# Kernel optimization log

Measured on AMD Instinct MI355X. Metric: run time of the kernel, lower is better.

The kernel has to match this reference:

```python
import jax, jax.numpy as jnp
import numpy as np

K_LO, K_HI = 5, 3
HAM_LO = jnp.asarray(np.outer(np.hamming(K_LO), np.hamming(K_LO)), dtype=jnp.float32)
HAM_HI = jnp.asarray(np.outer(np.hamming(K_HI), np.hamming(K_HI)), dtype=jnp.float32)


def conv2d(x, w, b, pad):
    y = jax.lax.conv_general_dilated(x, w, (1, 1), [(pad, pad), (pad, pad)],
                                     dimension_numbers=('NCHW', 'OIHW', 'NCHW'))
    return y + b[None, :, None, None]


def kernel_normalizer(mask, k, ham):
    # softmax over k*k, modulate by hamming window, renormalize to sum 1
    n, mc, h, w = mask.shape
    ch = mc // (k * k)
    m = jax.nn.softmax(mask.reshape(n, ch, k * k, h, w), axis=2)
    m = m.reshape(n, ch, k, k, h, w) * ham[None, None, :, :, None, None]
    m = m / m.sum(axis=(2, 3), keepdims=True)
    return m.reshape(n, mc, h, w)


def extract_patches(x, k):
    # (n,c,h,w) -> (n,c,k*k,h,w), zero-padded, row-major kernel order (matches CARAFE)
    n, c, h, w = x.shape
    p = k // 2
    xp = jnp.pad(x, ((0, 0), (0, 0), (p, p), (p, p)))
    return jnp.stack([xp[:, :, i:i + h, j:j + w] for i in range(k) for j in range(k)], axis=2)


def carafe(x, mask, k, group, up):
    # content-aware reassembly: mask is at (h*up, w*up); source pixel = out_pixel // up
    n, c, h, w = x.shape
    cg = c // group
    patches = extract_patches(x, k).reshape(n, group, cg, k * k, h, w)
    if up == 1:
        m = mask.reshape(n, group, k * k, h, w)
        return jnp.einsum('ngckhw,ngkhw->ngchw', patches, m).reshape(n, c, h, w)
    m = mask.reshape(n, group, k * k, h, up, w, up)
    out = jnp.einsum('ngckhw,ngkhuwv->ngchuwv', patches, m)
    return out.reshape(n, c, h * up, w * up)


def _forward(hr_feat, lr_feat, W_hr, b_hr, W_lr, b_lr, W_enc, b_enc, W_enc2, b_enc2):
    chf = conv2d(hr_feat, W_hr, b_hr, 0)
    clf = conv2d(lr_feat, W_lr, b_lr, 0)
    mask_hr_hr = conv2d(chf, W_enc2, b_enc2, 1)
    m_hi = kernel_normalizer(mask_hr_hr, K_HI, HAM_HI)
    chf = 2.0 * chf - carafe(chf, m_hi, K_HI, 1, 1)
    mask_lr_hr = conv2d(chf, W_enc, b_enc, 1)
    m_lo = kernel_normalizer(mask_lr_hr, K_LO, HAM_LO)
    # carafe(up=2) output is already at hr resolution -> F.interpolate(nearest) is identity
    mask_lr_lr = carafe(conv2d(clf, W_enc, b_enc, 1), m_lo, K_LO, 1, 2)
    mask_lr = mask_lr_hr + mask_lr_lr
    m_lo2 = kernel_normalizer(mask_lr, K_LO, HAM_LO)
    mask_hr_lr = carafe(conv2d(clf, W_enc2, b_enc2, 1), m_lo2, K_LO, 1, 2)
    mask_hr = mask_hr_hr + mask_hr_lr
    mask_lr_n = kernel_normalizer(mask_lr, K_LO, HAM_LO)
    lr_out = carafe(lr_feat, mask_lr_n, K_LO, 1, 2)
    mask_hr_n = kernel_normalizer(mask_hr, K_HI, HAM_HI)
    hr_out = 2.0 * hr_feat - carafe(hr_feat, mask_hr_n, K_HI, 1, 1)
    return (mask_lr_n, hr_out, lr_out)


def setup_inputs() -> dict:
    key = jax.random.key(0)
    ks = jax.random.split(key, 10)
    B, CHR, CLR, CC = 2, 256, 256, 64
    H, W = 128, 128
    h, w = H // 2, W // 2
    f32 = jnp.float32
    return {
        'hr_feat': jax.random.normal(ks[0], (B, CHR, H, W), f32),
        'lr_feat': jax.random.normal(ks[1], (B, CLR, h, w), f32),
        'W_hr': jax.random.normal(ks[2], (CC, CHR, 1, 1), f32) * 0.05,
        'b_hr': jnp.zeros((CC,), f32),
        'W_lr': jax.random.normal(ks[3], (CC, CLR, 1, 1), f32) * 0.05,
        'b_lr': jnp.zeros((CC,), f32),
        'W_enc': jax.random.normal(ks[4], (K_LO * K_LO, CC, 3, 3), f32) * 0.001,
        'b_enc': jnp.zeros((K_LO * K_LO,), f32),
        'W_enc2': jax.random.normal(ks[5], (K_HI * K_HI, CC, 3, 3), f32) * 0.001,
        'b_enc2': jnp.zeros((K_HI * K_HI,), f32),
    }


def reference(hr_feat, lr_feat, W_hr, b_hr, W_lr, b_lr, W_enc, b_enc, W_enc2, b_enc2):
    return _forward(hr_feat, lr_feat, W_hr, b_hr, W_lr, b_lr, W_enc, b_enc, W_enc2, b_enc2)
```

## Files before the change

### kernel.cpp

```cpp
#include <hip/hip_runtime.h>

#define HWH 16384
#define HWL 4096
#define WH 128
#define WL 64

__device__ __forceinline__ float ham3v(int t) {
    const float h[3] = {0.08f, 1.0f, 0.08f};
    return h[t / 3] * h[t % 3];
}
__device__ __forceinline__ float ham5v(int t) {
    const float h[5] = {0.08f, 0.54f, 1.0f, 0.54f, 0.08f};
    return h[t / 5] * h[t % 5];
}

template <int K>
__device__ __forceinline__ void normalize_post(float* m) {
    constexpr int K2 = K * K;
    float mx = -1e30f;
#pragma unroll
    for (int k = 0; k < K2; k++) mx = fmaxf(mx, m[k]);
    float s = 0.f;
#pragma unroll
    for (int k = 0; k < K2; k++) {
        float hv = (K == 3) ? ham3v(k) : ham5v(k);
        float e = __expf(m[k] - mx) * hv;
        m[k] = e;
        s += e;
    }
    float inv = 1.f / s;
#pragma unroll
    for (int k = 0; k < K2; k++) m[k] *= inv;
}

template <int K>
__device__ __forceinline__ void normalize_mask(const float* __restrict src, int stride,
                                               float* m) {
#pragma unroll
    for (int k = 0; k < K * K; k++) m[k] = src[(size_t)k * stride];
    normalize_post<K>(m);
}

struct F4 { float x, y, z, w; };
__device__ __forceinline__ F4 ld4u(const float* p) {
    F4 v;
    __builtin_memcpy(&v, p, 16);
    return v;
}

__device__ __forceinline__ float4 add4(float4 a, float4 b) {
    return make_float4(a.x + b.x, a.y + b.y, a.z + b.z, a.w + b.w);
}

__global__ void prep_w_k(const float* __restrict Whr, const float* __restrict Wlr,
                         const float* __restrict Wenc, const float* __restrict Wenc2,
                         float* __restrict wbase) {
    int tid = blockIdx.x * blockDim.x + threadIdx.x;
    int stride = gridDim.x * blockDim.x;
    float* wt_hr = wbase;
    float* wt_lr = wbase + 16384;
    float* wtE = wbase + 32768;
    float* wtE2 = wbase + 51200;
    for (int i = tid; i < 16384; i += stride) {
        int ci = i >> 6, co = i & 63;
        wt_hr[i] = Whr[co * 256 + ci];
        wt_lr[i] = Wlr[co * 256 + ci];
    }
    for (int i = tid; i < 18432; i += stride) {
        int r = i >> 5, co = i & 31;
        int ci = r / 9, t = r % 9;
        wtE[i] = (co < 25) ? Wenc[(co * 64 + ci) * 9 + t] : 0.f;
    }
    for (int i = tid; i < 9216; i += stride) {
        int r = i >> 4, co = i & 15;
        int ci = r / 9, t = r % 9;
        wtE2[i] = (co < 9) ? Wenc2[(co * 64 + ci) * 9 + t] : 0.f;
    }
}

__global__ __launch_bounds__(512) void conv1x1_all_k(
    const float* __restrict hr, const float* __restrict lrf, const float* __restrict wt_hr,
    const float* __restrict wt_lr, const float* __restrict bhr, const float* __restrict blr,
    float* __restrict chf, float* __restrict clf, int N) {
    __shared__ float sm[128 * 128];
    int b = blockIdx.x;
    const int HRB = (HWH / 128) * N;
    const float *x, *wt, *bias;
    float* y;
    int HWp, n, px0;
    if (b < HRB) {
        x = hr; wt = wt_hr; bias = bhr; y = chf; HWp = HWH;
        n = b / (HWH / 128);
        px0 = (b % (HWH / 128)) * 128;
    } else {
        int b2 = b - HRB;
        x = lrf; wt = wt_lr; bias = blr; y = clf; HWp = HWL;
        n = b2 / (HWL / 128);
        px0 = (b2 % (HWL / 128)) * 128;
    }
    const float* xb = x + (size_t)n * 256 * HWp + px0;
    int pl = threadIdx.x & 127;
    int co0 = __builtin_amdgcn_readfirstlane((int)(threadIdx.x >> 7)) * 16;
    float acc[16];
#pragma unroll
    for (int j = 0; j < 16; j++) acc[j] = 0.f;
    const float* w0 = wt + co0;
#pragma unroll
    for (int half = 0; half < 2; half++) {
        __syncthreads();
        for (int e = threadIdx.x; e < 4096; e += 512) {
            int ci = e >> 5, q = e & 31;
            *reinterpret_cast<float4*>(sm + ci * 128 + q * 4) =
                *reinterpret_cast<const float4*>(xb + (size_t)(half * 128 + ci) * HWp + q * 4);
        }
        __syncthreads();
        const float* wh = w0 + (half * 128) * 64;
#pragma unroll 8
        for (int ci = 0; ci < 128; ci++) {
            float xv = sm[ci * 128 + pl];
            const float* wr = wh + ci * 64;
#pragma unroll
            for (int j = 0; j < 16; j++) acc[j] = fmaf(wr[j], xv, acc[j]);
        }
    }
    float* yb = y + ((size_t)(n * 64 + co0)) * HWp + px0 + pl;
#pragma unroll
    for (int j = 0; j < 16; j++) yb[(size_t)j * HWp] = acc[j] + bias[co0 + j];
}

template <int COUT, int CH, int PAD, int LOG2W, int HH, int WW, int NCI>
__device__ __forceinline__ void conv3x3_2px(const float* __restrict x,
                                            const float* __restrict wt,
                                            const float* __restrict bias,
                                            float* __restrict y, int n, int g, int pxh,
                                            int ci0, bool addb) {
    constexpr int HWp = HH * WW;
    int px = pxh * 2;
    int yy = px >> LOG2W, xx = px & (WW - 1);
    int co0 = g * CH;
    float a0[CH], a1[CH];
#pragma unroll
    for (int j = 0; j < CH; j++) { a0[j] = 0.f; a1[j] = 0.f; }
    const float* xb = x + (size_t)(n * 64 + ci0) * HWp;
    const float* wb0 = wt + (size_t)ci0 * 9 * PAD + co0;
    int roff[3];
    bool rv[3];
#pragma unroll
    for (int r = 0; r < 3; r++) {
        int sy = yy + r - 1;
        rv[r] = (sy >= 0) && (sy < HH);
        roff[r] = sy * WW + xx - 1;
    }
    bool lv = (xx > 0), rgv = (xx < WW - 2);
    for (int ci = 0; ci < NCI; ci++) {
        const float* xc = xb + (size_t)ci * HWp;
        const float* w = wb0 + (size_t)ci * 9 * PAD;
#pragma unroll
        for (int r = 0; r < 3; r++) {
            F4 v = ld4u(xc + roff[r]);
            float t0 = (rv[r] && lv) ? v.x : 0.f;
            float t1 = rv[r] ? v.y : 0.f;
            float t2 = rv[r] ? v.z : 0.f;
            float t3 = (rv[r] && rgv) ? v.w : 0.f;
#pragma unroll
            for (int j = 0; j < CH; j++) {
                float w0 = w[(r * 3 + 0) * PAD + j];
                float w1 = w[(r * 3 + 1) * PAD + j];
                float w2 = w[(r * 3 + 2) * PAD + j];
                a0[j] = fmaf(w0, t0, fmaf(w1, t1, fmaf(w2, t2, a0[j])));
                a1[j] = fmaf(w0, t1, fmaf(w1, t2, fmaf(w2, t3, a1[j])));
            }
        }
    }
#pragma unroll
    for (int j = 0; j < CH; j++) {
        int co = co0 + j;
        if (co < COUT) {
            float bv = addb ? bias[co] : 0.f;
            float* op = y + ((size_t)(n * COUT + co)) * HWp + px;
            *reinterpret_cast<float2*>(op) = make_float2(a0[j] + bv, a1[j] + bv);
        }
    }
}

__global__ __launch_bounds__(256) void conv3x3_CGK_k(
    const float* __restrict chf, const float* __restrict clf, const float* __restrict wtE,
    const float* __restrict wtE2, const float* __restrict benc,
    const float* __restrict benc2, float* __restrict mh_P, float* __restrict g_P,
    float* __restrict k_P, int N) {
    const size_t MS = (size_t)N * 9 * HWH, GS = (size_t)N * 25 * HWL,
                 KS = (size_t)N * 9 * HWL;
    const int GBl = 8 * N * 5 * 4, KBl = 8 * N * 2 * 4;
    int b = blockIdx.x;
    if (b < GBl) {
        int pxb = b % 8;
        int n = (b / 8) % N;
        int t = b / (8 * N);
        int g = t % 5, s = t / 5;
        conv3x3_2px<25, 5, 32, 6, WL, WL, 16>(clf, wtE, benc, g_P + s * GS, n, g,
                                              pxb * 256 + (int)threadIdx.x, s * 16, s == 0);
    } else if (b < GBl + KBl) {
        int b2 = b - GBl;
        int pxb = b2 % 8;
        int n = (b2 / 8) % N;
        int t = b2 / (8 * N);
        int g = t % 2, s = t / 2;
        conv3x3_2px<9, 5, 16, 6, WL, WL, 16>(clf, wtE2, benc2, k_P + s * KS, n, g,
                                             pxb * 256 + (int)threadIdx.x, s * 16, s == 0);
    } else {
        int b3 = b - GBl - KBl;
        int pxb = b3 % 32;
        int n = (b3 / 32) % N;
        int t = b3 / (32 * N);
        int g = t % 3, s = t / 3;
        conv3x3_2px<9, 3, 16, 7, WH, WH, 16>(chf, wtE2, benc2, mh_P + s * MS, n, g,
                                             pxb * 256 + (int)threadIdx.x, s * 16, s == 0);
    }
}

__global__ __launch_bounds__(256) void conv3x3_F_k(const float* __restrict chf2,
                                                   const float* __restrict wtE,
                                                   const float* __restrict benc,
                                                   float* __restrict mlr_P, int N) {
    const size_t FS = (size_t)N * 25 * HWH;
    int t = blockIdx.x;
    int pxb = t % 32; t /= 32;
    int n = t % N; t /= N;
    int g = t % 5;
    int s = t / 5;
    conv3x3_2px<25, 5, 32, 7, WH, WH, 16>(chf2, wtE, benc, mlr_P + s * FS, n, g,
                                          pxb * 256 + (int)threadIdx.x, s * 16, s == 0);
}

__global__ void sum4n_gkc_k(const float* __restrict mh_P, float* __restrict mh_sum,
                            float* __restrict mh_n, const float4* __restrict g,
                            float4* __restrict g_d, const float4* __restrict k,
                            float4* __restrict k_d, int N) {
    const int NA = N * HWH / 256;
    const int E2 = N * 25 * HWL / 4, E3 = N * 9 * HWL / 4;
    const int NB = E2 / 256;
    const size_t MS = (size_t)N * 9 * HWH;
    int b = blockIdx.x;
    if (b < NA) {
        int lin = b * 256 + threadIdx.x;
        int n = lin / HWH, px = lin % HWH;
        float m[9];
#pragma unroll
        for (int c = 0; c < 9; c++) {
            size_t o = ((size_t)n * 9 + c) * HWH + px;
            float s = mh_P[o] + mh_P[o + MS] + mh_P[o + 2 * MS] + mh_P[o + 3 * MS];
            m[c] = s;
            mh_sum[o] = s;
        }
        normalize_post<3>(m);
#pragma unroll
        for (int c = 0; c < 9; c++) mh_n[((size_t)n * 9 + c) * HWH + px] = m[c];
    } else if (b < NA + NB) {
        int i = (b - NA) * 256 + threadIdx.x;
        if (i < E2) g_d[i] = add4(add4(g[i], g[i + E2]), add4(g[i + 2 * E2], g[i + 3 * E2]));
    } else {
        int i = (b - NA - NB) * 256 + threadIdx.x;
        if (i < E3) k_d[i] = add4(add4(k[i], k[i + E3]), add4(k[i + 2 * E3], k[i + 3 * E3]));
    }
}

__global__ void sum4fn_k(const float* __restrict p, float* __restrict sum,
                         float* __restrict nrm, int N) {
    int lin = blockIdx.x * 64 + threadIdx.x;
    int n = lin / HWH, px = lin % HWH;
    const size_t FS = (size_t)N * 25 * HWH;
    float m[25];
#pragma unroll
    for (int c = 0; c < 25; c++) {
        size_t o = ((size_t)n * 25 + c) * HWH + px;
        float s = p[o] + p[o + FS] + p[o + 2 * FS] + p[o + 3 * FS];
        sum[o] = s;
        m[c] = s;
    }
    normalize_post<5>(m);
    float* np = nrm + (size_t)n * 25 * HWH + px;
#pragma unroll
    for (int c = 0; c < 25; c++) np[(size_t)c * HWH] = m[c];
}

__device__ __forceinline__ void stage_tile18(const float* __restrict src,
                                             float (*__restrict tile)[18][136], int y0) {
    int tid = threadIdx.x;
    if (tid < 144) {
        int r = tid >> 3, c8 = tid & 7;
        int col = (c8 < 4) ? c8 : 128 + c8;
#pragma unroll
        for (int c = 0; c < 4; c++) tile[c][r][col] = 0.f;
    }
#pragma unroll
    for (int c = 0; c < 4; c++) {
        const float* sp = src + (size_t)c * HWH;
#pragma unroll
        for (int p = 0; p < 3; p++) {
            int e = tid + p * 256;
            if (e < 576) {
                int r = e >> 5, q = e & 31;
                int gy = y0 + r - 1;
                float4 v = make_float4(0.f, 0.f, 0.f, 0.f);
                if (gy >= 0 && gy < WH) v = *(const float4*)(sp + gy * WH + q * 4);
                *(float4*)&tile[c][r][4 + q * 4] = v;
            }
        }
    }
    __syncthreads();
}

template <bool SUBTRACT>
__device__ __forceinline__ void carafe3_tile8(const float (*__restrict tile)[18][136],
                                              const float* __restrict mb, int y0,
                                              float* __restrict ob) {
    int ly = threadIdx.x >> 4;
    int x0 = (threadIdx.x & 15) * 8;
    int px = (y0 + ly) * WH + x0;
    float4 ma[9], mbv[9];
#pragma unroll
    for (int t = 0; t < 9; t++) {
        ma[t] = *(const float4*)(mb + (size_t)t * HWH + px);
        mbv[t] = *(const float4*)(mb + (size_t)t * HWH + px + 4);
    }
    for (int c = 0; c < 4; c++) {
        float row[3][10];
#pragma unroll
        for (int r = 0; r < 3; r++) {
            const float* tp = &tile[c][ly + r][0];
            float lft = tp[3 + x0];
            float4 m0 = *(const float4*)&tp[4 + x0];
            float4 m1 = *(const float4*)&tp[8 + x0];
            float rgt = tp[12 + x0];
            row[r][0] = lft;
            row[r][1] = m0.x; row[r][2] = m0.y; row[r][3] = m0.z; row[r][4] = m0.w;
            row[r][5] = m1.x; row[r][6] = m1.y; row[r][7] = m1.z; row[r][8] = m1.w;
            row[r][9] = rgt;
        }
        float4 resA, resB;
        float* rp = &resA.x;
        float* rq = &resB.x;
#pragma unroll
        for (int p = 0; p < 8; p++) {
            float s = 0.f;
#pragma unroll
            for (int r = 0; r < 3; r++)
#pragma unroll
                for (int cc = 0; cc < 3; cc++) {
                    float mv = (p < 4) ? ((const float*)&ma[r * 3 + cc])[p]
                                       : ((const float*)&mbv[r * 3 + cc])[p - 4];
                    s = fmaf(mv, row[r][p + cc], s);
                }
            float o = SUBTRACT ? (2.f * row[1][p + 1] - s) : s;
            if (p < 4) rp[p] = o; else rq[p - 4] = o;
        }
        float* op = ob + (size_t)c * HWH + px;
        *(float4*)op = resA;
        *(float4*)(op + 4) = resB;
    }
}

__global__ __launch_bounds__(256) void fuse_de_k(const float* __restrict chf,
                                                 const float* __restrict m9n,
                                                 float* __restrict chf2, int N) {
    __shared__ float tile[4][18][136];
    int b = blockIdx.x;
    int yt = b & 7;
    int g = (b >> 3) & 15;
    int n = b >> 7;
    int y0 = yt * 16;
    int c0 = g * 4;
    stage_tile18(chf + ((size_t)n * 64 + c0) * HWH, tile, y0);
    carafe3_tile8<true>(tile, m9n + (size_t)n * 9 * HWH, y0,
                        chf2 + ((size_t)n * 64 + c0) * HWH);
}

__global__ void fuse_hi_k(const float* __restrict msum, const float* __restrict mn,
                          const float* __restrict g, float* __restrict mask_lr, int N) {
    int b = blockIdx.x;
    int pxb = b % 64;
    int n = (b / 64) % N;
    int co0 = (b / (64 * N)) * 5;
    int px = pxb * 256 + threadIdx.x;
    int Y = px >> 7, X = px & 127;
    int h = Y >> 1, w = X >> 1;
    const float* mb = msum + (size_t)n * 25 * HWH + px;
    const float* nb = mn + (size_t)n * 25 * HWH + px;
    float ml[25];
#pragma unroll
    for (int k = 0; k < 25; k++) ml[k] = nb[(size_t)k * HWH];
    float acc[5];
#pragma unroll
    for (int j = 0; j < 5; j++) acc[j] = 0.f;
    const float* gb = g + ((size_t)n * 25 + co0) * HWL;
    for (int k = 0; k < 25; k++) {
        int sy = h + k / 5 - 2, sx = w + k % 5 - 2;
        if (sy >= 0 && sy < WL && sx >= 0 && sx < WL) {
            int off = sy * WL + sx;
            float mk = ml[k];
#pragma unroll
            for (int j = 0; j < 5; j++)
                acc[j] = fmaf(mk, gb[(size_t)j * HWL + off], acc[j]);
        }
    }
#pragma unroll
    for (int j = 0; j < 5; j++)
        mask_lr[((size_t)(n * 25 + co0 + j)) * HWH + px] =
            mb[(size_t)(co0 + j) * HWH] + acc[j];
}

__global__ void fuse_l_norm_k(const float* __restrict mask_lr, const float* __restrict kf,
                              const float* __restrict mh_sum, float* __restrict out0,
                              float* __restrict mask_hr_n, int N) {
    int b = blockIdx.x;
    int px = (b % 256) * 64 + threadIdx.x;
    int n = b / 256;
    int Y = px >> 7, X = px & 127;
    int h = Y >> 1, w = X >> 1;
    float ml[25];
    normalize_mask<5>(mask_lr + (size_t)n * 25 * HWH + px, HWH, ml);
    float* op = out0 + (size_t)n * 25 * HWH + px;
#pragma unroll
    for (int k = 0; k < 25; k++) op[(size_t)k * HWH] = ml[k];
    float acc[9];
#pragma unroll
    for (int j = 0; j < 9; j++) acc[j] = 0.f;
    const float* kb = kf + (size_t)n * 9 * HWL;
    for (int k = 0; k < 25; k++) {
        int sy = h + k / 5 - 2, sx = w + k % 5 - 2;
        if (sy >= 0 && sy < WL && sx >= 0 && sx < WL) {
            int off = sy * WL + sx;
            float mk = ml[k];
#pragma unroll
            for (int j = 0; j < 9; j++)
                acc[j] = fmaf(mk, kb[(size_t)j * HWL + off], acc[j]);
        }
    }
    float mh[9];
#pragma unroll
    for (int j = 0; j < 9; j++)
        mh[j] = mh_sum[((size_t)(n * 9 + j)) * HWH + px] + acc[j];
    normalize_post<3>(mh);
    float* dp = mask_hr_n + (size_t)n * 9 * HWH + px;
#pragma unroll
    for (int j = 0; j < 9; j++) dp[(size_t)j * HWH] = mh[j];
}

__global__ __launch_bounds__(256) void hr_out_k(const float* __restrict m9n,
                                                const float* __restrict hr,
                                                float* __restrict out1, int N) {
    __shared__ float tile[4][18][136];
    int b = blockIdx.x;
    int yt = b & 7;
    int g = (b >> 3) & 63;
    int n = b >> 9;
    int y0 = yt * 16;
    int c0 = g * 4;
    stage_tile18(hr + ((size_t)n * 256 + c0) * HWH, tile, y0);
    carafe3_tile8<true>(tile, m9n + (size_t)n * 9 * HWH, y0,
                        out1 + ((size_t)n * 256 + c0) * HWH);
}

#define LRCHG 8
__global__ __launch_bounds__(256) void lr_out_k(const float* __restrict m_n,
                                                const float* __restrict lr,
                                                float* __restrict out2, int N) {
    __shared__ float tile[LRCHG][12][68];
    int b = blockIdx.x;
    int yt = b & 7;
    int g = (b >> 3) & 31;
    int n = b >> 8;
    int y0 = yt * 16;
    int hbase = y0 >> 1;
    int c0 = g * LRCHG;
    const float* lrb = lr + ((size_t)n * 256 + c0) * HWL;
    if (threadIdx.x < 48) {
        int r = threadIdx.x >> 2, c4 = threadIdx.x & 3;
        int col = (c4 < 2) ? c4 : 64 + c4;
#pragma unroll
        for (int c = 0; c < LRCHG; c++) tile[c][r][col] = 0.f;
    }
#pragma unroll
    for (int c = 0; c < LRCHG; c++) {
        const float* sp = lrb + (size_t)c * HWL;
#pragma unroll
        for (int p = 0; p < 2; p++) {
            int e = threadIdx.x + p * 256;
            if (e < 384) {
                int r = e >> 5, q = e & 31;
                int h = hbase + r - 2;
                float2 v = make_float2(0.f, 0.f);
                if (h >= 0 && h < WL) v = *(const float2*)(sp + h * WL + q * 2);
                *(float2*)&tile[c][r][2 + q * 2] = v;
            }
        }
    }
    __syncthreads();
    const float* mb = m_n + (size_t)n * 25 * HWH;
    float* ob = out2 + ((size_t)n * 256 + c0) * HWH;
#pragma unroll
    for (int i = 0; i < 2; i++) {
        int q = threadIdx.x + 256 * i;
        int qy = q >> 6, qx = q & 63;
        int Y0 = y0 + 2 * qy;
        int X0 = 2 * qx;
        float2 mk0[25], mk1[25];
#pragma unroll
        for (int k = 0; k < 25; k++) {
            mk0[k] = *(const float2*)(mb + (size_t)k * HWH + Y0 * WH + X0);
            mk1[k] = *(const float2*)(mb + (size_t)k * HWH + (Y0 + 1) * WH + X0);
        }
        for (int c = 0; c < LRCHG; c++) {
            float a00 = 0.f, a01 = 0.f, a10 = 0.f, a11 = 0.f;
#pragma unroll
            for (int k = 0; k < 25; k++) {
                float v = tile[c][qy + k / 5][qx + k % 5];
                a00 = fmaf(mk0[k].x, v, a00);
                a01 = fmaf(mk0[k].y, v, a01);
                a10 = fmaf(mk1[k].x, v, a10);
                a11 = fmaf(mk1[k].y, v, a11);
            }
            float* op = ob + (size_t)c * HWH + (size_t)Y0 * WH + X0;
            *(float2*)op = make_float2(a00, a01);
            *(float2*)(op + WH) = make_float2(a10, a11);
        }
    }
}

extern "C" void kernel_launch(void* const* d_in, const int* in_sizes, int n_in, void* d_out,
                              int out_size, void* d_ws, size_t ws_size, hipStream_t stream) {
    const float* hr = (const float*)d_in[0];
    const float* lr = (const float*)d_in[1];
    const float* Whr = (const float*)d_in[2];
    const float* bhr = (const float*)d_in[3];
    const float* Wlr = (const float*)d_in[4];
    const float* blr = (const float*)d_in[5];
    const float* Wenc = (const float*)d_in[6];
    const float* benc = (const float*)d_in[7];
    const float* Wenc2 = (const float*)d_in[8];
    const float* benc2 = (const float*)d_in[9];
    float* out = (float*)d_out;
    const int B = in_sizes[0] / (256 * HWH);
    (void)d_ws; (void)ws_size;

    float* out0 = out;
    float* O1 = out + (size_t)B * 25 * HWH;
    float* O2 = O1 + (size_t)B * 256 * HWH;

    const size_t MS = (size_t)B * 9 * HWH;
    const size_t GS = (size_t)B * 25 * HWL;
    const size_t KS = (size_t)B * 9 * HWL;
    const size_t FS = (size_t)B * 25 * HWH;

    float* wbase = O2;
    float* wt_hr = wbase;
    float* wt_lr = wbase + 16384;
    float* wtE = wbase + 32768;
    float* wtE2 = wbase + 51200;
    float* mh_P = O2 + 60416;
    float* g_P = mh_P + 4 * MS;
    float* k_P = g_P + 4 * GS;
    float* m_hrhr_sum = k_P + 4 * KS;
    float* g_sum = m_hrhr_sum + MS;
    float* k_sum = g_sum + GS;
    float* m_lrhr_sum = k_sum + KS;
    float* mask_hr_n = m_lrhr_sum + FS;
    float* m_lrhr_n = mask_hr_n + MS;

    float* chf = O1;
    float* chf2 = chf + (size_t)B * 64 * HWH;
    float* clf = chf2 + (size_t)B * 64 * HWH;
    float* mlr_P = clf + (size_t)B * 64 * HWL;
    float* m_hrhr_n = mlr_P + 4 * FS;
    float* mask_lr = mlr_P;

    prep_w_k<<<64, 256, 0, stream>>>(Whr, Wlr, Wenc, Wenc2, wbase);
    conv1x1_all_k<<<(HWH / 128) * B + (HWL / 128) * B, 512, 0, stream>>>(
        hr, lr, wt_hr, wt_lr, bhr, blr, chf, clf, B);
    conv3x3_CGK_k<<<8 * B * 5 * 4 + 8 * B * 2 * 4 + 32 * B * 3 * 4, 256, 0, stream>>>(
        chf, clf, wtE, wtE2, benc, benc2, mh_P, g_P, k_P, B);
    {
        int NA = B * HWH / 256;
        int NB = (B * 25 * HWL / 4) / 256, NC = (B * 9 * HWL / 4) / 256;
        sum4n_gkc_k<<<NA + NB + NC, 256, 0, stream>>>(
            mh_P, m_hrhr_sum, m_hrhr_n, (const float4*)g_P, (float4*)g_sum,
            (const float4*)k_P, (float4*)k_sum, B);
    }
    fuse_de_k<<<B * 128, 256, 0, stream>>>(chf, m_hrhr_n, chf2, B);
    conv3x3_F_k<<<32 * B * 5 * 4, 256, 0, stream>>>(chf2, wtE, benc, mlr_P, B);
    sum4fn_k<<<B * HWH / 64, 64, 0, stream>>>(mlr_P, m_lrhr_sum, m_lrhr_n, B);
    fuse_hi_k<<<64 * B * 5, 256, 0, stream>>>(m_lrhr_sum, m_lrhr_n, g_sum, mask_lr, B);
    fuse_l_norm_k<<<256 * B, 64, 0, stream>>>(mask_lr, k_sum, m_hrhr_sum, out0, mask_hr_n,
                                              B);
    hr_out_k<<<B * 512, 256, 0, stream>>>(mask_hr_n, hr, O1, B);
    lr_out_k<<<B * 256, 256, 0, stream>>>(out0, lr, O2, B);
}
```

Before: 159.2 us.

## Merge hr/lr output kernels into one launch; halve conv1x1 block size

The hr_out and lr_out carafe kernels are combined into a single launch that picks its branch from the block index. To make this safe, the normalized hr mask moves from the O2 region, which lr_out overwrites, into the workspace. The old two-kernel path stays as a fallback when the workspace is too small. Separately, conv1x1 now uses 256-thread blocks over 64 pixels instead of 512 threads over 128, which doubles the block count and halves shared memory per block, trading some weight reuse for more occupancy.

```diff
diff --git a/kernel.cpp b/kernel.cpp
--- a/kernel.cpp
+++ b/kernel.cpp
@@ -78,29 +78,29 @@
     }
 }
 
-__global__ __launch_bounds__(512) void conv1x1_all_k(
+__global__ __launch_bounds__(256) void conv1x1_all_k(
     const float* __restrict hr, const float* __restrict lrf, const float* __restrict wt_hr,
     const float* __restrict wt_lr, const float* __restrict bhr, const float* __restrict blr,
     float* __restrict chf, float* __restrict clf, int N) {
-    __shared__ float sm[128 * 128];
+    __shared__ float sm[128 * 64];
     int b = blockIdx.x;
-    const int HRB = (HWH / 128) * N;
+    const int HRB = (HWH / 64) * N;
     const float *x, *wt, *bias;
     float* y;
     int HWp, n, px0;
     if (b < HRB) {
         x = hr; wt = wt_hr; bias = bhr; y = chf; HWp = HWH;
-        n = b / (HWH / 128);
-        px0 = (b % (HWH / 128)) * 128;
+        n = b / (HWH / 64);
+        px0 = (b % (HWH / 64)) * 64;
     } else {
         int b2 = b - HRB;
         x = lrf; wt = wt_lr; bias = blr; y = clf; HWp = HWL;
-        n = b2 / (HWL / 128);
-        px0 = (b2 % (HWL / 128)) * 128;
+        n = b2 / (HWL / 64);
+        px0 = (b2 % (HWL / 64)) * 64;
     }
     const float* xb = x + (size_t)n * 256 * HWp + px0;
-    int pl = threadIdx.x & 127;
-    int co0 = __builtin_amdgcn_readfirstlane((int)(threadIdx.x >> 7)) * 16;
+    int pl = threadIdx.x & 63;
+    int co0 = __builtin_amdgcn_readfirstlane((int)(threadIdx.x >> 6)) * 16;
     float acc[16];
 #pragma unroll
     for (int j = 0; j < 16; j++) acc[j] = 0.f;
@@ -108,16 +108,16 @@
 #pragma unroll
     for (int half = 0; half < 2; half++) {
         __syncthreads();
-        for (int e = threadIdx.x; e < 4096; e += 512) {
-            int ci = e >> 5, q = e & 31;
-            *reinterpret_cast<float4*>(sm + ci * 128 + q * 4) =
+        for (int e = threadIdx.x; e < 2048; e += 256) {
+            int ci = e >> 4, q = e & 15;
+            *reinterpret_cast<float4*>(sm + ci * 64 + q * 4) =
                 *reinterpret_cast<const float4*>(xb + (size_t)(half * 128 + ci) * HWp + q * 4);
         }
         __syncthreads();
         const float* wh = w0 + (half * 128) * 64;
 #pragma unroll 8
         for (int ci = 0; ci < 128; ci++) {
-            float xv = sm[ci * 128 + pl];
+            float xv = sm[ci * 64 + pl];
             const float* wr = wh + ci * 64;
 #pragma unroll
             for (int j = 0; j < 16; j++) acc[j] = fmaf(wr[j], xv, acc[j]);
@@ -360,6 +360,87 @@
     }
 }
 
+__device__ __forceinline__ void hr_out_body(float* __restrict smem,
+                                            const float* __restrict m9n,
+                                            const float* __restrict hr,
+                                            float* __restrict out1, int b, int N) {
+    float(*tile)[18][136] = reinterpret_cast<float(*)[18][136]>(smem);
+    int yt = b & 7;
+    int g = (b >> 3) & 63;
+    int n = b >> 9;
+    int y0 = yt * 16;
+    int c0 = g * 4;
+    stage_tile18(hr + ((size_t)n * 256 + c0) * HWH, tile, y0);
+    carafe3_tile8<true>(tile, m9n + (size_t)n * 9 * HWH, y0,
+                        out1 + ((size_t)n * 256 + c0) * HWH);
+}
+
+#define LRCHG 8
+__device__ __forceinline__ void lr_out_body(float* __restrict smem,
+                                            const float* __restrict m_n,
+                                            const float* __restrict lrf,
+                                            float* __restrict out2, int b, int N) {
+    float(*tile)[12][68] = reinterpret_cast<float(*)[12][68]>(smem);
+    int yt = b & 7;
+    int g = (b >> 3) & 31;
+    int n = b >> 8;
+    int y0 = yt * 16;
+    int hbase = y0 >> 1;
+    int c0 = g * LRCHG;
+    const float* lrb = lrf + ((size_t)n * 256 + c0) * HWL;
+    if (threadIdx.x < 48) {
+        int r = threadIdx.x >> 2, c4 = threadIdx.x & 3;
+        int col = (c4 < 2) ? c4 : 64 + c4;
+#pragma unroll
+        for (int c = 0; c < LRCHG; c++) tile[c][r][col] = 0.f;
+    }
+#pragma unroll
+    for (int c = 0; c < LRCHG; c++) {
+        const float* sp = lrb + (size_t)c * HWL;
+#pragma unroll
+        for (int p = 0; p < 2; p++) {
+            int e = threadIdx.x + p * 256;
+            if (e < 384) {
+                int r = e >> 5, q = e & 31;
+                int h = hbase + r - 2;
+                float2 v = make_float2(0.f, 0.f);
+                if (h >= 0 && h < WL) v = *(const float2*)(sp + h * WL + q * 2);
+                *(float2*)&tile[c][r][2 + q * 2] = v;
+            }
+        }
+    }
+    __syncthreads();
+    const float* mb = m_n + (size_t)n * 25 * HWH;
+    float* ob = out2 + ((size_t)n * 256 + c0) * HWH;
+#pragma unroll
+    for (int i = 0; i < 2; i++) {
+        int q = threadIdx.x + 256 * i;
+        int qy = q >> 6, qx = q & 63;
+        int Y0 = y0 + 2 * qy;
+        int X0 = 2 * qx;
+        float2 mk0[25], mk1[25];
+#pragma unroll
+        for (int k = 0; k < 25; k++) {
+            mk0[k] = *(const float2*)(mb + (size_t)k * HWH + Y0 * WH + X0);
+            mk1[k] = *(const float2*)(mb + (size_t)k * HWH + (Y0 + 1) * WH + X0);
+        }
+        for (int c = 0; c < LRCHG; c++) {
+            float a00 = 0.f, a01 = 0.f, a10 = 0.f, a11 = 0.f;
+#pragma unroll
+            for (int k = 0; k < 25; k++) {
+                float v = tile[c][qy + k / 5][qx + k % 5];
+                a00 = fmaf(mk0[k].x, v, a00);
+                a01 = fmaf(mk0[k].y, v, a01);
+                a10 = fmaf(mk1[k].x, v, a10);
+                a11 = fmaf(mk1[k].y, v, a11);
+            }
+            float* op = ob + (size_t)c * HWH + (size_t)Y0 * WH + X0;
+            *(float2*)op = make_float2(a00, a01);
+            *(float2*)(op + WH) = make_float2(a10, a11);
+        }
+    }
+}
+
 __global__ __launch_bounds__(256) void fuse_de_k(const float* __restrict chf,
                                                  const float* __restrict m9n,
                                                  float* __restrict chf2, int N) {
@@ -449,81 +530,30 @@
 __global__ __launch_bounds__(256) void hr_out_k(const float* __restrict m9n,
                                                 const float* __restrict hr,
                                                 float* __restrict out1, int N) {
-    __shared__ float tile[4][18][136];
+    __shared__ float smem[4 * 18 * 136];
+    hr_out_body(smem, m9n, hr, out1, blockIdx.x, N);
+}
+
+__global__ __launch_bounds__(256) void lr_out_k(const float* __restrict m_n,
+                                                const float* __restrict lrf,
+                                                float* __restrict out2, int N) {
+    __shared__ float smem[LRCHG * 12 * 68];
+    lr_out_body(smem, m_n, lrf, out2, blockIdx.x, N);
+}
+
+__global__ __launch_bounds__(256) void hrlr_out_k(const float* __restrict m9n,
+                                                  const float* __restrict hr,
+                                                  float* __restrict out1,
+                                                  const float* __restrict m_n,
+                                                  const float* __restrict lrf,
+                                                  float* __restrict out2, int N) {
+    __shared__ float smem[4 * 18 * 136];
     int b = blockIdx.x;
-    int yt = b & 7;
-    int g = (b >> 3) & 63;
-    int n = b >> 9;
-    int y0 = yt * 16;
-    int c0 = g * 4;
-    stage_tile18(hr + ((size_t)n * 256 + c0) * HWH, tile, y0);
-    carafe3_tile8<true>(tile, m9n + (size_t)n * 9 * HWH, y0,
-                        out1 + ((size_t)n * 256 + c0) * HWH);
-}
-
-#define LRCHG 8
-__global__ __launch_bounds__(256) void lr_out_k(const float* __restrict m_n,
-                                                const float* __restrict lr,
-                                                float* __restrict out2, int N) {
-    __shared__ float tile[LRCHG][12][68];
-    int b = blockIdx.x;
-    int yt = b & 7;
-    int g = (b >> 3) & 31;
-    int n = b >> 8;
-    int y0 = yt * 16;
-    int hbase = y0 >> 1;
-    int c0 = g * LRCHG;
-    const float* lrb = lr + ((size_t)n * 256 + c0) * HWL;
-    if (threadIdx.x < 48) {
-        int r = threadIdx.x >> 2, c4 = threadIdx.x & 3;
-        int col = (c4 < 2) ? c4 : 64 + c4;
-#pragma unroll
-        for (int c = 0; c < LRCHG; c++) tile[c][r][col] = 0.f;
-    }
-#pragma unroll
-    for (int c = 0; c < LRCHG; c++) {
-        const float* sp = lrb + (size_t)c * HWL;
-#pragma unroll
-        for (int p = 0; p < 2; p++) {
-            int e = threadIdx.x + p * 256;
-            if (e < 384) {
-                int r = e >> 5, q = e & 31;
-                int h = hbase + r - 2;
-                float2 v = make_float2(0.f, 0.f);
-                if (h >= 0 && h < WL) v = *(const float2*)(sp + h * WL + q * 2);
-                *(float2*)&tile[c][r][2 + q * 2] = v;
-            }
-        }
-    }
-    __syncthreads();
-    const float* mb = m_n + (size_t)n * 25 * HWH;
-    float* ob = out2 + ((size_t)n * 256 + c0) * HWH;
-#pragma unroll
-    for (int i = 0; i < 2; i++) {
-        int q = threadIdx.x + 256 * i;
-        int qy = q >> 6, qx = q & 63;
-        int Y0 = y0 + 2 * qy;
-        int X0 = 2 * qx;
-        float2 mk0[25], mk1[25];
-#pragma unroll
-        for (int k = 0; k < 25; k++) {
-            mk0[k] = *(const float2*)(mb + (size_t)k * HWH + Y0 * WH + X0);
-            mk1[k] = *(const float2*)(mb + (size_t)k * HWH + (Y0 + 1) * WH + X0);
-        }
-        for (int c = 0; c < LRCHG; c++) {
-            float a00 = 0.f, a01 = 0.f, a10 = 0.f, a11 = 0.f;
-#pragma unroll
-            for (int k = 0; k < 25; k++) {
-                float v = tile[c][qy + k / 5][qx + k % 5];
-                a00 = fmaf(mk0[k].x, v, a00);
-                a01 = fmaf(mk0[k].y, v, a01);
-                a10 = fmaf(mk1[k].x, v, a10);
-                a11 = fmaf(mk1[k].y, v, a11);
-            }
-            float* op = ob + (size_t)c * HWH + (size_t)Y0 * WH + X0;
-            *(float2*)op = make_float2(a00, a01);
-            *(float2*)(op + WH) = make_float2(a10, a11);
-        }
+    const int HRB = N * 512;
+    if (b < HRB) {
+        hr_out_body(smem, m9n, hr, out1, b, N);
+    } else {
+        lr_out_body(smem, m_n, lrf, out2, b - HRB, N);
     }
 }
 
@@ -541,7 +571,6 @@
     const float* benc2 = (const float*)d_in[9];
     float* out = (float*)d_out;
     const int B = in_sizes[0] / (256 * HWH);
-    (void)d_ws; (void)ws_size;
 
     float* out0 = out;
     float* O1 = out + (size_t)B * 25 * HWH;
@@ -564,8 +593,8 @@
     float* g_sum = m_hrhr_sum + MS;
     float* k_sum = g_sum + GS;
     float* m_lrhr_sum = k_sum + KS;
-    float* mask_hr_n = m_lrhr_sum + FS;
-    float* m_lrhr_n = mask_hr_n + MS;
+    float* mask_hr_n_o2 = m_lrhr_sum + FS;
+    float* m_lrhr_n = mask_hr_n_o2 + MS;
 
     float* chf = O1;
     float* chf2 = chf + (size_t)B * 64 * HWH;
@@ -574,8 +603,11 @@
     float* m_hrhr_n = mlr_P + 4 * FS;
     float* mask_lr = mlr_P;
 
+    const bool use_ws = ws_size >= MS * sizeof(float);
+    float* mask_hr_n = use_ws ? (float*)d_ws : mask_hr_n_o2;
+
     prep_w_k<<<64, 256, 0, stream>>>(Whr, Wlr, Wenc, Wenc2, wbase);
-    conv1x1_all_k<<<(HWH / 128) * B + (HWL / 128) * B, 512, 0, stream>>>(
+    conv1x1_all_k<<<(HWH / 64) * B + (HWL / 64) * B, 256, 0, stream>>>(
         hr, lr, wt_hr, wt_lr, bhr, blr, chf, clf, B);
     conv3x3_CGK_k<<<8 * B * 5 * 4 + 8 * B * 2 * 4 + 32 * B * 3 * 4, 256, 0, stream>>>(
         chf, clf, wtE, wtE2, benc, benc2, mh_P, g_P, k_P, B);
@@ -592,6 +624,11 @@
     fuse_hi_k<<<64 * B * 5, 256, 0, stream>>>(m_lrhr_sum, m_lrhr_n, g_sum, mask_lr, B);
     fuse_l_norm_k<<<256 * B, 64, 0, stream>>>(mask_lr, k_sum, m_hrhr_sum, out0, mask_hr_n,
                                               B);
-    hr_out_k<<<B * 512, 256, 0, stream>>>(mask_hr_n, hr, O1, B);
-    lr_out_k<<<B * 256, 256, 0, stream>>>(out0, lr, O2, B);
-}
+    if (use_ws) {
+        hrlr_out_k<<<B * 512 + B * 256, 256, 0, stream>>>(mask_hr_n, hr, O1, out0, lr, O2,
+                                                          B);
+    } else {
+        hr_out_k<<<B * 512, 256, 0, stream>>>(mask_hr_n, hr, O1, B);
+        lr_out_k<<<B * 256, 256, 0, stream>>>(out0, lr, O2, B);
+    }
+}
```

Result: faster. 152.6 us (-4.2%).
